# Performance work log

Hardware: AMD Instinct MI355X
Metric: run time of the kernel (lower is better)

Reference implementation:

```python
import jax, jax.numpy as jnp
import numpy as np

S, C, K = 1024, 4096, 4


def setup_inputs() -> dict:
    key = jax.random.key(0)
    ks = jax.random.split(key, 12)
    log_delta = jax.random.normal(ks[0], (), dtype=jnp.float32)
    log_tau = jax.random.normal(ks[1], (), dtype=jnp.float32)
    log_lambda = jax.random.normal(ks[2], (), dtype=jnp.float32)
    # extinction probs in (0,1)
    E = jax.random.uniform(ks[3], (S,), dtype=jnp.float32, minval=0.01, maxval=0.9)
    # log conditional clade probabilities (finite, roughly log-prob scale)
    log_Pi = jax.random.normal(ks[4], (C, S), dtype=jnp.float32) - 2.0
    s_C1 = jax.random.randint(ks[5], (S,), 0, S, dtype=jnp.int32)
    s_C2 = jax.random.randint(ks[6], (S,), 0, S, dtype=jnp.int32)
    recip = (jax.random.uniform(ks[7], (S, S)) < 0.05).astype(jnp.float32)
    recip = jnp.maximum(recip, jnp.eye(S, dtype=jnp.float32))  # every node has >=1 recipient
    splits_c1 = jax.random.randint(ks[8], (C, K), 0, C, dtype=jnp.int32)
    splits_c2 = jax.random.randint(ks[9], (C, K), 0, C, dtype=jnp.int32)
    log_q = jax.nn.log_softmax(jax.random.normal(ks[10], (C, K), dtype=jnp.float32), axis=-1)
    is_leaf = jax.random.uniform(ks[11], (C,)) < 0.25
    return {
        'log_delta': log_delta, 'log_tau': log_tau, 'log_lambda': log_lambda,
        'E': E, 'log_Pi': log_Pi, 's_C1': s_C1, 's_C2': s_C2,
        'Recipients_mat': recip, 'splits_c1': splits_c1, 'splits_c2': splits_c2,
        'log_q': log_q, 'is_leaf': is_leaf, 'root_id': 0,
    }


def reference(log_delta, log_tau, log_lambda, E, log_Pi, s_C1, s_C2,
              Recipients_mat, splits_c1, splits_c2, log_q, is_leaf, root_id):
    # rates via softplus, event probabilities
    delta = jax.nn.softplus(log_delta)
    tau = jax.nn.softplus(log_tau)
    lam = jax.nn.softplus(log_lambda)
    rs = 1.0 + delta + tau + lam
    p_S, p_D, p_T, p_L = 1.0 / rs, delta / rs, tau / rs, lam / rs

    # ---- E-step: single Jacobi update of extinction probabilities ----
    cnt = jnp.maximum(Recipients_mat.sum(axis=1), 1.0)           # [S]
    Ebar = (Recipients_mat @ E) / cnt                            # [S] mean over recipients
    E_new = p_L + p_D * E * E + p_T * E * Ebar + p_S * E[s_C1] * E[s_C2]

    # ---- Pi update in log space (Jacobi over clades x species) ----
    lpS, lpD, lpT = jnp.log(p_S), jnp.log(p_D), jnp.log(p_T)
    # log mean of Pi over transfer recipients: logTbar [C,S]
    m = jnp.max(log_Pi, axis=1, keepdims=True)                   # [C,1]
    sums = jnp.exp(log_Pi - m) @ Recipients_mat.T                # [C,S]
    logTbar = jnp.log(jnp.maximum(sums, 1e-30)) - jnp.log(cnt)[None, :] + m

    A = log_Pi[splits_c1]                                        # [C,K,S] child-clade 1
    B = log_Pi[splits_c2]                                        # [C,K,S] child-clade 2
    Af, Ag = A[:, :, s_C1], A[:, :, s_C2]                        # gather species children
    Bf, Bg = B[:, :, s_C1], B[:, :, s_C2]
    lq = log_q[:, :, None]
    # speciation: children go to the two species children (both orders)
    spec = lpS + jax.nn.logsumexp(lq + jnp.logaddexp(Af + Bg, Ag + Bf), axis=1)
    # duplication: both children stay on species s
    dup = lpD + jax.nn.logsumexp(lq + A + B, axis=1)
    # transfer: one child stays, the other goes to a recipient (averaged)
    TbA, TbB = logTbar[splits_c1], logTbar[splits_c2]            # [C,K,S]
    trans = lpT + jax.nn.logsumexp(lq + jnp.logaddexp(A + TbB, B + TbA), axis=1)
    # speciation-loss: clade follows one species child, other lineage goes extinct
    logE = jnp.log(E_new)                                        # E_new > 0 (p_L > 0)
    sl = lpS + jnp.logaddexp(log_Pi[:, s_C1] + logE[s_C2][None, :],
                             log_Pi[:, s_C2] + logE[s_C1][None, :])
    combined = jax.nn.logsumexp(jnp.stack([spec, dup, trans, sl], axis=0), axis=0)
    log_Pi_new = jnp.where(is_leaf[:, None], log_Pi, combined)

    # log-likelihood at the root clade
    return jax.nn.logsumexp(log_Pi_new[root_id])
```

## Files before the change

kernel.cpp:

```cpp
#include <hip/hip_runtime.h>
#include <math.h>

#define S 1024
#define C 4096
#define K 4

__device__ __forceinline__ float softplusf(float x) {
    return fmaxf(x, 0.0f) + log1pf(expf(-fabsf(x)));
}
__device__ __forceinline__ float logaddexpf_(float a, float b) {
    float mx = fmaxf(a, b), mn = fminf(a, b);
    return mx + log1pf(expf(mn - mx));
}

__global__ __launch_bounds__(256) void k_ebar(
    const float* __restrict__ E, const float* __restrict__ Recip,
    const int* __restrict__ sC1, const int* __restrict__ sC2,
    const float* __restrict__ ld, const float* __restrict__ lt,
    const float* __restrict__ ll,
    float* __restrict__ logE, float* __restrict__ logCnt) {
    __shared__ float sc[256], sd[256];
    int j = blockIdx.x;
    int t = threadIdx.x;
    const float* row = Recip + (size_t)j * S;
    float c = 0.f, d = 0.f;
    for (int k = t; k < S; k += 256) {
        float r = row[k];
        c += r;
        d += r * E[k];
    }
    sc[t] = c; sd[t] = d;
    __syncthreads();
    for (int o = 128; o > 0; o >>= 1) {
        if (t < o) { sc[t] += sc[t + o]; sd[t] += sd[t + o]; }
        __syncthreads();
    }
    if (t == 0) {
        float cnt  = fmaxf(sc[0], 1.0f);
        float ebar = sd[0] / cnt;
        float delta = softplusf(ld[0]);
        float tau   = softplusf(lt[0]);
        float lam   = softplusf(ll[0]);
        float rs = 1.0f + delta + tau + lam;
        float pS = 1.0f / rs, pD = delta / rs, pT = tau / rs, pL = lam / rs;
        float Ej = E[j];
        float en = pL + pD * Ej * Ej + pT * Ej * ebar + pS * E[sC1[j]] * E[sC2[j]];
        logE[j]   = logf(en);
        logCnt[j] = logf(cnt);
    }
}

__global__ __launch_bounds__(1024) void k_wrow(
    const float* __restrict__ logPi, const int* __restrict__ sp1,
    const int* __restrict__ sp2, const int* __restrict__ rootp,
    float* __restrict__ wrows, float* __restrict__ mvals) {
    __shared__ float sm[1024];
    int slot = blockIdx.x;
    int t = threadIdx.x;
    int root = rootp[0];
    int row = (slot < K) ? sp1[root * K + slot] : sp2[root * K + (slot - K)];
    float v = logPi[(size_t)row * S + t];
    sm[t] = v;
    __syncthreads();
    for (int o = 512; o > 0; o >>= 1) {
        if (t < o) sm[t] = fmaxf(sm[t], sm[t + o]);
        __syncthreads();
    }
    float m = sm[0];
    wrows[slot * S + t] = expf(v - m);
    if (t == 0) mvals[slot] = m;
}

__global__ __launch_bounds__(256) void k_sums(
    const float* __restrict__ Recip, const float* __restrict__ wrows,
    const float* __restrict__ mvals, const float* __restrict__ logCnt,
    float* __restrict__ logTbar) {
    __shared__ float sa[256];
    int j = blockIdx.x, slot = blockIdx.y, t = threadIdx.x;
    const float* row = Recip + (size_t)j * S;
    const float* w = wrows + slot * S;
    float acc = 0.f;
    for (int k = t; k < S; k += 256) acc += row[k] * w[k];
    sa[t] = acc;
    __syncthreads();
    for (int o = 128; o > 0; o >>= 1) {
        if (t < o) sa[t] += sa[t + o];
        __syncthreads();
    }
    if (t == 0)
        logTbar[slot * S + j] = logf(fmaxf(sa[0], 1e-30f)) - logCnt[j] + mvals[slot];
}

__global__ __launch_bounds__(1024) void k_final(
    const float* __restrict__ logPi, const int* __restrict__ sC1,
    const int* __restrict__ sC2, const int* __restrict__ sp1,
    const int* __restrict__ sp2, const float* __restrict__ logq,
    const void* __restrict__ isLeaf, const int* __restrict__ rootp,
    const float* __restrict__ ld, const float* __restrict__ lt,
    const float* __restrict__ ll,
    const float* __restrict__ logE, const float* __restrict__ logTbar,
    float* __restrict__ out) {
    __shared__ float sA[8][S];
    __shared__ float sLogE[S];
    __shared__ float sRoot[S];
    __shared__ float red[1024];
    int t = threadIdx.x;
    int root = rootp[0];

    for (int slot = 0; slot < 8; ++slot) {
        int row = (slot < K) ? sp1[root * K + slot] : sp2[root * K + (slot - K)];
        sA[slot][t] = logPi[(size_t)row * S + t];
    }
    sLogE[t] = logE[t];
    sRoot[t] = logPi[(size_t)root * S + t];
    __syncthreads();

    float delta = softplusf(ld[0]);
    float tau   = softplusf(lt[0]);
    float lam   = softplusf(ll[0]);
    float rs = 1.0f + delta + tau + lam;
    float lpS = logf(1.0f / rs), lpD = logf(delta / rs), lpT = logf(tau / rs);

    int j = t;
    int f = sC1[j], g = sC2[j];

    float vs[K], vd[K], vt[K];
    float ms = -INFINITY, md = -INFINITY, mt = -INFINITY;
    for (int k = 0; k < K; ++k) {
        float lq = logq[root * K + k];
        float Aj = sA[k][j],     Bj = sA[4 + k][j];
        float Af = sA[k][f],     Ag = sA[k][g];
        float Bf = sA[4 + k][f], Bg = sA[4 + k][g];
        vs[k] = lq + logaddexpf_(Af + Bg, Ag + Bf);
        vd[k] = lq + Aj + Bj;
        float TbAj = logTbar[k * S + j];
        float TbBj = logTbar[(4 + k) * S + j];
        vt[k] = lq + logaddexpf_(Aj + TbBj, Bj + TbAj);
        ms = fmaxf(ms, vs[k]); md = fmaxf(md, vd[k]); mt = fmaxf(mt, vt[k]);
    }
    float ss = 0.f, sd_ = 0.f, st = 0.f;
    for (int k = 0; k < K; ++k) {
        ss  += expf(vs[k] - ms);
        sd_ += expf(vd[k] - md);
        st  += expf(vt[k] - mt);
    }
    float vspec  = lpS + ms + logf(ss);
    float vdup   = lpD + md + logf(sd_);
    float vtrans = lpT + mt + logf(st);
    float vsl = lpS + logaddexpf_(sRoot[f] + sLogE[g], sRoot[g] + sLogE[f]);

    float cm = fmaxf(fmaxf(vspec, vdup), fmaxf(vtrans, vsl));
    float comb = cm + logf(expf(vspec - cm) + expf(vdup - cm) +
                           expf(vtrans - cm) + expf(vsl - cm));

    unsigned int u = ((const unsigned int*)isLeaf)[root];
    bool leaf = ((u & 0xFFu) != 0u) || (u == 0x3F800000u);

    float x = leaf ? sRoot[j] : comb;

    red[t] = x;
    __syncthreads();
    for (int o = 512; o > 0; o >>= 1) {
        if (t < o) red[t] = fmaxf(red[t], red[t + o]);
        __syncthreads();
    }
    float m = red[0];
    __syncthreads();
    red[t] = expf(x - m);
    __syncthreads();
    for (int o = 512; o > 0; o >>= 1) {
        if (t < o) red[t] += red[t + o];
        __syncthreads();
    }
    if (t == 0) out[0] = m + logf(red[0]);
}

extern "C" void kernel_launch(void* const* d_in, const int* in_sizes, int n_in,
                              void* d_out, int out_size, void* d_ws, size_t ws_size,
                              hipStream_t stream) {
    const float* log_delta = (const float*)d_in[0];
    const float* log_tau   = (const float*)d_in[1];
    const float* log_lambda= (const float*)d_in[2];
    const float* E         = (const float*)d_in[3];
    const float* log_Pi    = (const float*)d_in[4];
    const int*   s_C1      = (const int*)d_in[5];
    const int*   s_C2      = (const int*)d_in[6];
    const float* Recip     = (const float*)d_in[7];
    const int*   splits_c1 = (const int*)d_in[8];
    const int*   splits_c2 = (const int*)d_in[9];
    const float* log_q     = (const float*)d_in[10];
    const void*  is_leaf   = (const void*)d_in[11];
    const int*   root_id   = (const int*)d_in[12];
    float* out = (float*)d_out;

    float* ws      = (float*)d_ws;
    float* logE    = ws;
    float* logCnt  = ws + S;
    float* wrows   = ws + 2 * S;
    float* mvals   = ws + 10 * S;
    float* logTbar = ws + 10 * S + 8;

    k_ebar<<<dim3(S), dim3(256), 0, stream>>>(E, Recip, s_C1, s_C2,
                                              log_delta, log_tau, log_lambda,
                                              logE, logCnt);
    k_wrow<<<dim3(8), dim3(1024), 0, stream>>>(log_Pi, splits_c1, splits_c2,
                                               root_id, wrows, mvals);
    k_sums<<<dim3(S, 8), dim3(256), 0, stream>>>(Recip, wrows, mvals, logCnt,
                                                 logTbar);
    k_final<<<dim3(1), dim3(1024), 0, stream>>>(log_Pi, s_C1, s_C2,
                                                splits_c1, splits_c2, log_q,
                                                is_leaf, root_id,
                                                log_delta, log_tau, log_lambda,
                                                logE, logTbar, out);
}
```

Before: 120.6 us.

## Fuse E-bar, weight-row and recipient-sum kernels into one wave-per-row kernel

Merges the three kernels that computed Ebar/logE, the exp-normalised root split rows, and the eight recipient-weighted sums into one kernel. Each block stages the 8 split rows and E in shared memory and recomputes the row maxima and exponentials locally. Each wave then reads one Recip row once with float4 loads and accumulates the count, the E dot product and all 8 slot sums together, finishing with shuffle reductions. This removes two launches and the 8-fold re-reading of Recip. In exchange every block redundantly loads and exponentiates the 8 rows.

```diff
diff --git a/kernel.cpp b/kernel.cpp
--- a/kernel.cpp
+++ b/kernel.cpp
@@ -4,6 +4,7 @@
 #define S 1024
 #define C 4096
 #define K 4
+#define NSLOT 8
 
 __device__ __forceinline__ float softplusf(float x) {
     return fmaxf(x, 0.0f) + log1pf(expf(-fabsf(x)));
@@ -12,83 +13,99 @@
     float mx = fmaxf(a, b), mn = fminf(a, b);
     return mx + log1pf(expf(mn - mx));
 }
-
-__global__ __launch_bounds__(256) void k_ebar(
-    const float* __restrict__ E, const float* __restrict__ Recip,
+__device__ __forceinline__ float wave_sum64(float v) {
+    for (int o = 32; o > 0; o >>= 1) v += __shfl_down(v, o, 64);
+    return v;
+}
+__device__ __forceinline__ float wave_max64(float v) {
+    for (int o = 32; o > 0; o >>= 1) v = fmaxf(v, __shfl_down(v, o, 64));
+    return v;
+}
+
+__global__ __launch_bounds__(256) void k_main(
+    const float* __restrict__ E, const float* __restrict__ logPi,
+    const float* __restrict__ Recip,
     const int* __restrict__ sC1, const int* __restrict__ sC2,
+    const int* __restrict__ sp1, const int* __restrict__ sp2,
+    const int* __restrict__ rootp,
     const float* __restrict__ ld, const float* __restrict__ lt,
     const float* __restrict__ ll,
-    float* __restrict__ logE, float* __restrict__ logCnt) {
-    __shared__ float sc[256], sd[256];
-    int j = blockIdx.x;
+    float* __restrict__ logE, float* __restrict__ logTbar) {
+    __shared__ __align__(16) float w[NSLOT][S];
+    __shared__ __align__(16) float els[S];
+    __shared__ float msh[NSLOT];
     int t = threadIdx.x;
-    const float* row = Recip + (size_t)j * S;
-    float c = 0.f, d = 0.f;
-    for (int k = t; k < S; k += 256) {
-        float r = row[k];
-        c += r;
-        d += r * E[k];
-    }
-    sc[t] = c; sd[t] = d;
-    __syncthreads();
-    for (int o = 128; o > 0; o >>= 1) {
-        if (t < o) { sc[t] += sc[t + o]; sd[t] += sd[t + o]; }
-        __syncthreads();
-    }
-    if (t == 0) {
-        float cnt  = fmaxf(sc[0], 1.0f);
-        float ebar = sd[0] / cnt;
+    int root = rootp[0];
+
+    for (int slot = 0; slot < NSLOT; ++slot) {
+        int row = (slot < K) ? sp1[root * K + slot] : sp2[root * K + (slot - K)];
+        const float* src = logPi + (size_t)row * S;
+        for (int k = t; k < S; k += 256) w[slot][k] = src[k];
+    }
+    for (int k = t; k < S; k += 256) els[k] = E[k];
+    __syncthreads();
+
+    int wave = t >> 6, lane = t & 63;
+    for (int s2 = 0; s2 < 2; ++s2) {
+        int slot = wave * 2 + s2;
+        float m = -INFINITY;
+        for (int k = lane; k < S; k += 64) m = fmaxf(m, w[slot][k]);
+        m = wave_max64(m);
+        if (lane == 0) msh[slot] = m;
+    }
+    __syncthreads();
+    for (int slot = 0; slot < NSLOT; ++slot) {
+        float m = msh[slot];
+        for (int k = t; k < S; k += 256) w[slot][k] = expf(w[slot][k] - m);
+    }
+    __syncthreads();
+
+    int j = blockIdx.x * 4 + wave;
+    const float4* rrow = (const float4*)(Recip + (size_t)j * S);
+    const float4* ev4 = (const float4*)els;
+    float4 aw[NSLOT];
+    float4 ac = make_float4(0.f, 0.f, 0.f, 0.f);
+    float4 ae = make_float4(0.f, 0.f, 0.f, 0.f);
+#pragma unroll
+    for (int s = 0; s < NSLOT; ++s) aw[s] = make_float4(0.f, 0.f, 0.f, 0.f);
+
+#pragma unroll
+    for (int i0 = 0; i0 < S / 4; i0 += 64) {
+        int i = i0 + lane;
+        float4 r = rrow[i];
+        float4 e = ev4[i];
+        ac.x += r.x; ac.y += r.y; ac.z += r.z; ac.w += r.w;
+        ae.x += r.x * e.x; ae.y += r.y * e.y; ae.z += r.z * e.z; ae.w += r.w * e.w;
+#pragma unroll
+        for (int s = 0; s < NSLOT; ++s) {
+            float4 wv = ((const float4*)w[s])[i];
+            aw[s].x += r.x * wv.x; aw[s].y += r.y * wv.y;
+            aw[s].z += r.z * wv.z; aw[s].w += r.w * wv.w;
+        }
+    }
+    float c = wave_sum64(ac.x + ac.y + ac.z + ac.w);
+    float ed = wave_sum64(ae.x + ae.y + ae.z + ae.w);
+    float as[NSLOT];
+#pragma unroll
+    for (int s = 0; s < NSLOT; ++s)
+        as[s] = wave_sum64(aw[s].x + aw[s].y + aw[s].z + aw[s].w);
+
+    if (lane == 0) {
+        float cnt = fmaxf(c, 1.0f);
+        float logCnt = logf(cnt);
+#pragma unroll
+        for (int s = 0; s < NSLOT; ++s)
+            logTbar[s * S + j] = logf(fmaxf(as[s], 1e-30f)) - logCnt + msh[s];
         float delta = softplusf(ld[0]);
-        float tau   = softplusf(lt[0]);
-        float lam   = softplusf(ll[0]);
+        float tau = softplusf(lt[0]);
+        float lam = softplusf(ll[0]);
         float rs = 1.0f + delta + tau + lam;
         float pS = 1.0f / rs, pD = delta / rs, pT = tau / rs, pL = lam / rs;
-        float Ej = E[j];
-        float en = pL + pD * Ej * Ej + pT * Ej * ebar + pS * E[sC1[j]] * E[sC2[j]];
-        logE[j]   = logf(en);
-        logCnt[j] = logf(cnt);
-    }
-}
-
-__global__ __launch_bounds__(1024) void k_wrow(
-    const float* __restrict__ logPi, const int* __restrict__ sp1,
-    const int* __restrict__ sp2, const int* __restrict__ rootp,
-    float* __restrict__ wrows, float* __restrict__ mvals) {
-    __shared__ float sm[1024];
-    int slot = blockIdx.x;
-    int t = threadIdx.x;
-    int root = rootp[0];
-    int row = (slot < K) ? sp1[root * K + slot] : sp2[root * K + (slot - K)];
-    float v = logPi[(size_t)row * S + t];
-    sm[t] = v;
-    __syncthreads();
-    for (int o = 512; o > 0; o >>= 1) {
-        if (t < o) sm[t] = fmaxf(sm[t], sm[t + o]);
-        __syncthreads();
-    }
-    float m = sm[0];
-    wrows[slot * S + t] = expf(v - m);
-    if (t == 0) mvals[slot] = m;
-}
-
-__global__ __launch_bounds__(256) void k_sums(
-    const float* __restrict__ Recip, const float* __restrict__ wrows,
-    const float* __restrict__ mvals, const float* __restrict__ logCnt,
-    float* __restrict__ logTbar) {
-    __shared__ float sa[256];
-    int j = blockIdx.x, slot = blockIdx.y, t = threadIdx.x;
-    const float* row = Recip + (size_t)j * S;
-    const float* w = wrows + slot * S;
-    float acc = 0.f;
-    for (int k = t; k < S; k += 256) acc += row[k] * w[k];
-    sa[t] = acc;
-    __syncthreads();
-    for (int o = 128; o > 0; o >>= 1) {
-        if (t < o) sa[t] += sa[t + o];
-        __syncthreads();
-    }
-    if (t == 0)
-        logTbar[slot * S + j] = logf(fmaxf(sa[0], 1e-30f)) - logCnt[j] + mvals[slot];
+        float Ej = els[j];
+        float en = pL + pD * Ej * Ej + pT * Ej * (ed / cnt)
+                 + pS * els[sC1[j]] * els[sC2[j]];
+        logE[j] = logf(en);
+    }
 }
 
 __global__ __launch_bounds__(1024) void k_final(
@@ -100,14 +117,14 @@
     const float* __restrict__ ll,
     const float* __restrict__ logE, const float* __restrict__ logTbar,
     float* __restrict__ out) {
-    __shared__ float sA[8][S];
+    __shared__ float sA[NSLOT][S];
     __shared__ float sLogE[S];
     __shared__ float sRoot[S];
     __shared__ float red[1024];
     int t = threadIdx.x;
     int root = rootp[0];
 
-    for (int slot = 0; slot < 8; ++slot) {
+    for (int slot = 0; slot < NSLOT; ++slot) {
         int row = (slot < K) ? sp1[root * K + slot] : sp2[root * K + (slot - K)];
         sA[slot][t] = logPi[(size_t)row * S + t];
     }
@@ -116,8 +133,8 @@
     __syncthreads();
 
     float delta = softplusf(ld[0]);
-    float tau   = softplusf(lt[0]);
-    float lam   = softplusf(ll[0]);
+    float tau = softplusf(lt[0]);
+    float lam = softplusf(ll[0]);
     float rs = 1.0f + delta + tau + lam;
     float lpS = logf(1.0f / rs), lpD = logf(delta / rs), lpT = logf(tau / rs);
 
@@ -126,10 +143,11 @@
 
     float vs[K], vd[K], vt[K];
     float ms = -INFINITY, md = -INFINITY, mt = -INFINITY;
+#pragma unroll
     for (int k = 0; k < K; ++k) {
         float lq = logq[root * K + k];
-        float Aj = sA[k][j],     Bj = sA[4 + k][j];
-        float Af = sA[k][f],     Ag = sA[k][g];
+        float Aj = sA[k][j], Bj = sA[4 + k][j];
+        float Af = sA[k][f], Ag = sA[k][g];
         float Bf = sA[4 + k][f], Bg = sA[4 + k][g];
         vs[k] = lq + logaddexpf_(Af + Bg, Ag + Bf);
         vd[k] = lq + Aj + Bj;
@@ -139,13 +157,14 @@
         ms = fmaxf(ms, vs[k]); md = fmaxf(md, vd[k]); mt = fmaxf(mt, vt[k]);
     }
     float ss = 0.f, sd_ = 0.f, st = 0.f;
+#pragma unroll
     for (int k = 0; k < K; ++k) {
-        ss  += expf(vs[k] - ms);
+        ss += expf(vs[k] - ms);
         sd_ += expf(vd[k] - md);
-        st  += expf(vt[k] - mt);
-    }
-    float vspec  = lpS + ms + logf(ss);
-    float vdup   = lpD + md + logf(sd_);
+        st += expf(vt[k] - mt);
+    }
+    float vspec = lpS + ms + logf(ss);
+    float vdup = lpD + md + logf(sd_);
     float vtrans = lpT + mt + logf(st);
     float vsl = lpS + logaddexpf_(sRoot[f] + sLogE[g], sRoot[g] + sLogE[f]);
 
@@ -155,7 +174,6 @@
 
     unsigned int u = ((const unsigned int*)isLeaf)[root];
     bool leaf = ((u & 0xFFu) != 0u) || (u == 0x3F800000u);
-
     float x = leaf ? sRoot[j] : comb;
 
     red[t] = x;
@@ -179,37 +197,28 @@
                               void* d_out, int out_size, void* d_ws, size_t ws_size,
                               hipStream_t stream) {
     const float* log_delta = (const float*)d_in[0];
-    const float* log_tau   = (const float*)d_in[1];
-    const float* log_lambda= (const float*)d_in[2];
-    const float* E         = (const float*)d_in[3];
-    const float* log_Pi    = (const float*)d_in[4];
-    const int*   s_C1      = (const int*)d_in[5];
-    const int*   s_C2      = (const int*)d_in[6];
-    const float* Recip     = (const float*)d_in[7];
-    const int*   splits_c1 = (const int*)d_in[8];
-    const int*   splits_c2 = (const int*)d_in[9];
-    const float* log_q     = (const float*)d_in[10];
-    const void*  is_leaf   = (const void*)d_in[11];
-    const int*   root_id   = (const int*)d_in[12];
+    const float* log_tau = (const float*)d_in[1];
+    const float* log_lambda = (const float*)d_in[2];
+    const float* E = (const float*)d_in[3];
+    const float* log_Pi = (const float*)d_in[4];
+    const int* s_C1 = (const int*)d_in[5];
+    const int* s_C2 = (const int*)d_in[6];
+    const float* Recip = (const float*)d_in[7];
+    const int* splits_c1 = (const int*)d_in[8];
+    const int* splits_c2 = (const int*)d_in[9];
+    const float* log_q = (const float*)d_in[10];
+    const void* is_leaf = (const void*)d_in[11];
+    const int* root_id = (const int*)d_in[12];
     float* out = (float*)d_out;
 
-    float* ws      = (float*)d_ws;
-    float* logE    = ws;
-    float* logCnt  = ws + S;
-    float* wrows   = ws + 2 * S;
-    float* mvals   = ws + 10 * S;
-    float* logTbar = ws + 10 * S + 8;
-
-    k_ebar<<<dim3(S), dim3(256), 0, stream>>>(E, Recip, s_C1, s_C2,
-                                              log_delta, log_tau, log_lambda,
-                                              logE, logCnt);
-    k_wrow<<<dim3(8), dim3(1024), 0, stream>>>(log_Pi, splits_c1, splits_c2,
-                                               root_id, wrows, mvals);
-    k_sums<<<dim3(S, 8), dim3(256), 0, stream>>>(Recip, wrows, mvals, logCnt,
-                                                 logTbar);
-    k_final<<<dim3(1), dim3(1024), 0, stream>>>(log_Pi, s_C1, s_C2,
-                                                splits_c1, splits_c2, log_q,
-                                                is_leaf, root_id,
-                                                log_delta, log_tau, log_lambda,
-                                                logE, logTbar, out);
-}
+    float* ws = (float*)d_ws;
+    float* logE = ws;
+    float* logTbar = ws + S;
+
+    k_main<<<dim3(S / 4), dim3(256), 0, stream>>>(
+        E, log_Pi, Recip, s_C1, s_C2, splits_c1, splits_c2, root_id,
+        log_delta, log_tau, log_lambda, logE, logTbar);
+    k_final<<<dim3(1), dim3(1024), 0, stream>>>(
+        log_Pi, s_C1, s_C2, splits_c1, splits_c2, log_q, is_leaf, root_id,
+        log_delta, log_tau, log_lambda, logE, logTbar, out);
+}
```

Measured after the change: 122.4 us. No clear change (+1.5%).
